# Kernel tuning notes

Measured on AMD Instinct MI355X. Metric: run time of the kernel, lower is better.

Reference implementation:

```python
import jax, jax.numpy as jnp
import numpy as np

BLOCK = 4096
V, D = 50304, 1024
EPS = 1e-5


def setup_inputs() -> dict:
    key = jax.random.key(0)
    k1, k2, k3, k4, k5, k6 = jax.random.split(key, 6)
    x = jax.random.randint(k1, (8, 2048), 0, V, dtype=jnp.int64)
    weight_i8 = jax.random.randint(k2, (V, D), 0, 256, dtype=jnp.int32)
    absmax = jax.random.uniform(k3, (V * D // BLOCK,), dtype=jnp.float32)
    code = jax.random.normal(k4, (256,), dtype=jnp.float32)
    ln_weight = jax.random.uniform(k5, (D,), dtype=jnp.float32)
    ln_bias = jax.random.normal(k6, (D,), dtype=jnp.float32)
    return {"x": x, "weight_i8": weight_i8, "absmax": absmax, "code": code,
            "ln_weight": ln_weight, "ln_bias": ln_bias}


def reference(x, weight_i8, absmax, code, ln_weight, ln_bias):
    # Blockwise dequant of the FULL table (faithful to the original forward):
    # each flat block of BLOCK elements shares one absmax scale;
    # int8 codes index a 256-entry code table.
    deq = code[weight_i8.reshape(-1, BLOCK)] * absmax[:, None]   # [nblocks, BLOCK]
    weight_deq = deq.reshape(V, D)
    emb = weight_deq[x]                                           # [B, S, D] gather
    # LayerNorm over the embedding dim with affine params
    mean = jnp.mean(emb, axis=-1, keepdims=True)
    var = jnp.mean(jnp.square(emb - mean), axis=-1, keepdims=True)
    normed = (emb - mean) * jax.lax.rsqrt(var + EPS)
    return normed * ln_weight + ln_bias
```

## Files before the change

kernel.cpp:

```cpp
#include <hip/hip_runtime.h>

#define D 1024
#define EPS 1e-5f

__global__ __launch_bounds__(256) void emb_deq_ln_kernel(
    const int*   __restrict__ x,
    const int*   __restrict__ w,
    const float* __restrict__ absmax,
    const float* __restrict__ code,
    const float* __restrict__ ln_w,
    const float* __restrict__ ln_b,
    float*       __restrict__ out)
{
    __shared__ float code_s[256];
    __shared__ float red[8];
    __shared__ float stats[2];

    const int tid = threadIdx.x;

    code_s[tid] = code[tid];

    const int t = blockIdx.x;
    const int v = x[t];
    const float scale = absmax[v >> 2];

    const int4 wq = ((const int4*)(w + (size_t)v * D))[tid];

    __syncthreads();

    float vals[4];
    vals[0] = code_s[wq.x] * scale;
    vals[1] = code_s[wq.y] * scale;
    vals[2] = code_s[wq.z] * scale;
    vals[3] = code_s[wq.w] * scale;

    float s  = vals[0] + vals[1] + vals[2] + vals[3];
    float ss = vals[0]*vals[0] + vals[1]*vals[1] + vals[2]*vals[2] + vals[3]*vals[3];

    #pragma unroll
    for (int off = 32; off > 0; off >>= 1) {
        s  += __shfl_down(s,  off, 64);
        ss += __shfl_down(ss, off, 64);
    }
    const int lane = tid & 63;
    const int wid  = tid >> 6;
    if (lane == 0) { red[wid * 2] = s; red[wid * 2 + 1] = ss; }
    __syncthreads();

    if (tid == 0) {
        const float ts  = red[0] + red[2] + red[4] + red[6];
        const float tss = red[1] + red[3] + red[5] + red[7];
        const float mean = ts * (1.0f / D);
        const float var  = tss * (1.0f / D) - mean * mean;
        stats[0] = mean;
        stats[1] = rsqrtf(var + EPS);
    }
    __syncthreads();

    const float mean = stats[0];
    const float rstd = stats[1];

    const float4 lw = ((const float4*)ln_w)[tid];
    const float4 lb = ((const float4*)ln_b)[tid];

    float4 o;
    o.x = (vals[0] - mean) * rstd * lw.x + lb.x;
    o.y = (vals[1] - mean) * rstd * lw.y + lb.y;
    o.z = (vals[2] - mean) * rstd * lw.z + lb.z;
    o.w = (vals[3] - mean) * rstd * lw.w + lb.w;

    ((float4*)(out + (size_t)t * D))[tid] = o;
}

extern "C" void kernel_launch(void* const* d_in, const int* in_sizes, int n_in,
                              void* d_out, int out_size, void* d_ws, size_t ws_size,
                              hipStream_t stream) {
    const int*   x      = (const int*)d_in[0];
    const int*   w      = (const int*)d_in[1];
    const float* absmax = (const float*)d_in[2];
    const float* code   = (const float*)d_in[3];
    const float* ln_w   = (const float*)d_in[4];
    const float* ln_b   = (const float*)d_in[5];
    float* out = (float*)d_out;

    const int T = in_sizes[0];

    emb_deq_ln_kernel<<<T, 256, 0, stream>>>(x, w, absmax, code, ln_w, ln_b, out);
}
```

Measured before the change: 278.4 us.

## Map one wavefront per token row with shuffle-only reduction and nontemporal stores

Each 256-thread block now handles four tokens, one wavefront per row, with every lane covering 16 elements. The LayerNorm statistics come from an xor-shuffle reduction inside the wavefront, which removes the shared-memory reduction and two block barriers. Output is written with nontemporal stores to avoid polluting cache. This cuts the block count by four and raises per-thread register use and memory-level parallelism, but each block still loads the code table and passes one barrier.

```diff
diff --git a/kernel.cpp b/kernel.cpp
--- a/kernel.cpp
+++ b/kernel.cpp
@@ -2,6 +2,8 @@
 
 #define D 1024
 #define EPS 1e-5f
+
+typedef float v4f __attribute__((ext_vector_type(4)));
 
 __global__ __launch_bounds__(256) void emb_deq_ln_kernel(
     const int*   __restrict__ x,
@@ -10,66 +12,86 @@
     const float* __restrict__ code,
     const float* __restrict__ ln_w,
     const float* __restrict__ ln_b,
-    float*       __restrict__ out)
+    float*       __restrict__ out,
+    int T)
 {
     __shared__ float code_s[256];
-    __shared__ float red[8];
-    __shared__ float stats[2];
 
-    const int tid = threadIdx.x;
+    const int tid  = threadIdx.x;
+    const int lane = tid & 63;
+    const int wid  = tid >> 6;
 
     code_s[tid] = code[tid];
 
-    const int t = blockIdx.x;
-    const int v = x[t];
+    int t = blockIdx.x * 4 + wid;
+    t = min(t, T - 1);
+
+    const int   v     = x[t];
     const float scale = absmax[v >> 2];
 
-    const int4 wq = ((const int4*)(w + (size_t)v * D))[tid];
+    const int4* __restrict__ wrow = (const int4*)(w + (size_t)v * D);
+    const int4 q0 = wrow[lane];
+    const int4 q1 = wrow[lane + 64];
+    const int4 q2 = wrow[lane + 128];
+    const int4 q3 = wrow[lane + 192];
+
+    const float4* lw4 = (const float4*)ln_w;
+    const float4* lb4 = (const float4*)ln_b;
+    const float4 lw0 = lw4[lane];       const float4 lb0 = lb4[lane];
+    const float4 lw1 = lw4[lane + 64];  const float4 lb1 = lb4[lane + 64];
+    const float4 lw2 = lw4[lane + 128]; const float4 lb2 = lb4[lane + 128];
+    const float4 lw3 = lw4[lane + 192]; const float4 lb3 = lb4[lane + 192];
 
     __syncthreads();
 
-    float vals[4];
-    vals[0] = code_s[wq.x] * scale;
-    vals[1] = code_s[wq.y] * scale;
-    vals[2] = code_s[wq.z] * scale;
-    vals[3] = code_s[wq.w] * scale;
+    float4 v0, v1, v2, v3;
+    v0.x = code_s[q0.x] * scale; v0.y = code_s[q0.y] * scale;
+    v0.z = code_s[q0.z] * scale; v0.w = code_s[q0.w] * scale;
+    v1.x = code_s[q1.x] * scale; v1.y = code_s[q1.y] * scale;
+    v1.z = code_s[q1.z] * scale; v1.w = code_s[q1.w] * scale;
+    v2.x = code_s[q2.x] * scale; v2.y = code_s[q2.y] * scale;
+    v2.z = code_s[q2.z] * scale; v2.w = code_s[q2.w] * scale;
+    v3.x = code_s[q3.x] * scale; v3.y = code_s[q3.y] * scale;
+    v3.z = code_s[q3.z] * scale; v3.w = code_s[q3.w] * scale;
 
-    float s  = vals[0] + vals[1] + vals[2] + vals[3];
-    float ss = vals[0]*vals[0] + vals[1]*vals[1] + vals[2]*vals[2] + vals[3]*vals[3];
+    float s  = (v0.x + v0.y + v0.z + v0.w) + (v1.x + v1.y + v1.z + v1.w)
+             + (v2.x + v2.y + v2.z + v2.w) + (v3.x + v3.y + v3.z + v3.w);
+    float ss = (v0.x*v0.x + v0.y*v0.y + v0.z*v0.z + v0.w*v0.w)
+             + (v1.x*v1.x + v1.y*v1.y + v1.z*v1.z + v1.w*v1.w)
+             + (v2.x*v2.x + v2.y*v2.y + v2.z*v2.z + v2.w*v2.w)
+             + (v3.x*v3.x + v3.y*v3.y + v3.z*v3.z + v3.w*v3.w);
 
     #pragma unroll
     for (int off = 32; off > 0; off >>= 1) {
-        s  += __shfl_down(s,  off, 64);
-        ss += __shfl_down(ss, off, 64);
+        s  += __shfl_xor(s,  off, 64);
+        ss += __shfl_xor(ss, off, 64);
     }
-    const int lane = tid & 63;
-    const int wid  = tid >> 6;
-    if (lane == 0) { red[wid * 2] = s; red[wid * 2 + 1] = ss; }
-    __syncthreads();
 
-    if (tid == 0) {
-        const float ts  = red[0] + red[2] + red[4] + red[6];
-        const float tss = red[1] + red[3] + red[5] + red[7];
-        const float mean = ts * (1.0f / D);
-        const float var  = tss * (1.0f / D) - mean * mean;
-        stats[0] = mean;
-        stats[1] = rsqrtf(var + EPS);
-    }
-    __syncthreads();
+    const float mean = s * (1.0f / D);
+    const float rstd = rsqrtf(ss * (1.0f / D) - mean * mean + EPS);
 
-    const float mean = stats[0];
-    const float rstd = stats[1];
-
-    const float4 lw = ((const float4*)ln_w)[tid];
-    const float4 lb = ((const float4*)ln_b)[tid];
-
-    float4 o;
-    o.x = (vals[0] - mean) * rstd * lw.x + lb.x;
-    o.y = (vals[1] - mean) * rstd * lw.y + lb.y;
-    o.z = (vals[2] - mean) * rstd * lw.z + lb.z;
-    o.w = (vals[3] - mean) * rstd * lw.w + lb.w;
-
-    ((float4*)(out + (size_t)t * D))[tid] = o;
+    v4f* orow = (v4f*)(out + (size_t)t * D);
+    v4f o;
+    o.x = (v0.x - mean) * rstd * lw0.x + lb0.x;
+    o.y = (v0.y - mean) * rstd * lw0.y + lb0.y;
+    o.z = (v0.z - mean) * rstd * lw0.z + lb0.z;
+    o.w = (v0.w - mean) * rstd * lw0.w + lb0.w;
+    __builtin_nontemporal_store(o, &orow[lane]);
+    o.x = (v1.x - mean) * rstd * lw1.x + lb1.x;
+    o.y = (v1.y - mean) * rstd * lw1.y + lb1.y;
+    o.z = (v1.z - mean) * rstd * lw1.z + lb1.z;
+    o.w = (v1.w - mean) * rstd * lw1.w + lb1.w;
+    __builtin_nontemporal_store(o, &orow[lane + 64]);
+    o.x = (v2.x - mean) * rstd * lw2.x + lb2.x;
+    o.y = (v2.y - mean) * rstd * lw2.y + lb2.y;
+    o.z = (v2.z - mean) * rstd * lw2.z + lb2.z;
+    o.w = (v2.w - mean) * rstd * lw2.w + lb2.w;
+    __builtin_nontemporal_store(o, &orow[lane + 128]);
+    o.x = (v3.x - mean) * rstd * lw3.x + lb3.x;
+    o.y = (v3.y - mean) * rstd * lw3.y + lb3.y;
+    o.z = (v3.z - mean) * rstd * lw3.z + lb3.z;
+    o.w = (v3.w - mean) * rstd * lw3.w + lb3.w;
+    __builtin_nontemporal_store(o, &orow[lane + 192]);
 }
 
 extern "C" void kernel_launch(void* const* d_in, const int* in_sizes, int n_in,
@@ -85,5 +107,6 @@
 
     const int T = in_sizes[0];
 
-    emb_deq_ln_kernel<<<T, 256, 0, stream>>>(x, w, absmax, code, ln_w, ln_b, out);
+    const int grid = (T + 3) / 4;
+    emb_deq_ln_kernel<<<grid, 256, 0, stream>>>(x, w, absmax, code, ln_w, ln_b, out, T);
 }
```

After: 278.7 us. About the same (+0.1%).
